# Kernel tuning notes

Measured on AMD Instinct MI355X. Metric: run time of the kernel, lower is better.

## Reference

```python
import jax, jax.numpy as jnp
import numpy as np

B = 8192
INPUT_DIM = 1024
PATH_DIM = 256
HIDDEN_DIM = 1024
OUTPUT_DIM = 1024
STEPS = 50


def setup_inputs() -> dict:
    key = jax.random.key(0)
    ks = jax.random.split(key, 12)
    s = lambda fan_in: 1.0 / np.sqrt(fan_in)
    x0 = jax.random.normal(ks[0], (B, INPUT_DIM), dtype=jnp.float32)
    W_pe = jax.random.uniform(ks[1], (INPUT_DIM, PATH_DIM), jnp.float32, -s(INPUT_DIM), s(INPUT_DIM))
    b_pe = jax.random.uniform(ks[2], (PATH_DIM,), jnp.float32, -s(INPUT_DIM), s(INPUT_DIM))
    W_hi = jax.random.uniform(ks[3], (INPUT_DIM, HIDDEN_DIM), jnp.float32, -s(INPUT_DIM), s(INPUT_DIM))
    b_hi = jax.random.uniform(ks[4], (HIDDEN_DIM,), jnp.float32, -s(INPUT_DIM), s(INPUT_DIM))
    f_in = HIDDEN_DIM + PATH_DIM
    W1 = jax.random.uniform(ks[5], (f_in, HIDDEN_DIM), jnp.float32, -s(f_in), s(f_in))
    b1 = jax.random.uniform(ks[6], (HIDDEN_DIM,), jnp.float32, -s(f_in), s(f_in))
    W2 = jax.random.uniform(ks[7], (HIDDEN_DIM, HIDDEN_DIM), jnp.float32, -s(HIDDEN_DIM), s(HIDDEN_DIM))
    b2 = jax.random.uniform(ks[8], (HIDDEN_DIM,), jnp.float32, -s(HIDDEN_DIM), s(HIDDEN_DIM))
    W_ro = jax.random.uniform(ks[9], (HIDDEN_DIM, OUTPUT_DIM), jnp.float32, -s(HIDDEN_DIM), s(HIDDEN_DIM))
    b_ro = jax.random.uniform(ks[10], (OUTPUT_DIM,), jnp.float32, -s(HIDDEN_DIM), s(HIDDEN_DIM))
    return {"x0": x0, "W_pe": W_pe, "b_pe": b_pe, "W_hi": W_hi, "b_hi": b_hi,
            "W1": W1, "b1": b1, "W2": W2, "b2": b2, "W_ro": W_ro, "b_ro": b_ro}


def reference(x0, W_pe, b_pe, W_hi, b_hi, W1, b1, W2, b2, W_ro, b_ro):
    dt = 1.0 / float(STEPS)
    g = x0 @ W_pe + b_pe          # [B, path_dim]
    z0 = x0 @ W_hi + b_hi          # [B, hidden_dim]
    ts = dt * jnp.arange(1, STEPS + 1, dtype=jnp.float32)  # t after each step

    def step(z, t):
        u_t = t * g                                  # [B, path_dim]
        inp = jnp.concatenate([z, u_t], axis=-1)     # [B, hidden+path]
        dz = jnp.tanh(inp @ W1 + b1) @ W2 + b2       # [B, hidden_dim]
        return z + dt * dz, None

    z, _ = jax.lax.scan(step, z0, ts)
    return z @ W_ro + b_ro
```

## Files before the change

### kernel.cpp

```cpp
#include <hip/hip_runtime.h>
#include <hip/hip_bf16.h>

typedef __hip_bfloat16 bf16;
typedef __bf16 bf16x8 __attribute__((ext_vector_type(8)));
typedef float f32x4 __attribute__((ext_vector_type(4)));

#define ROWS   32
#define HID    1024
#define PATH   256
#define NSTEP  50
#define P      1032
#define SMEM_BYTES (2 * ROWS * P * 2)

__device__ __forceinline__ f32x4 mfma16(bf16x8 a, bf16x8 b, f32x4 c) {
    return __builtin_amdgcn_mfma_f32_16x16x32_bf16(a, b, c, 0, 0, 0);
}

__device__ __forceinline__ float tanh_fast(float x) {
    float e = __expf(2.0f * x);
    return 1.0f - 2.0f / (e + 1.0f);
}

__device__ __forceinline__ bf16x8 ldcvt8(const float* __restrict__ p) {
    f32x4 lo = *(const f32x4*)p;
    f32x4 hi = *(const f32x4*)(p + 4);
    bf16x8 r;
    #pragma unroll
    for (int j = 0; j < 4; j++) { r[j] = (__bf16)lo[j]; r[4 + j] = (__bf16)hi[j]; }
    return r;
}

__global__ void pack_frag(const float* __restrict__ src, bf16* __restrict__ dst, int N) {
    int kb = blockIdx.x, nb = blockIdx.y, l = threadIdx.x;
    int lm = l & 15, lq = l >> 4;
    bf16x8 v;
    #pragma unroll
    for (int j = 0; j < 8; j++)
        v[j] = __float2bfloat16(src[(size_t)(kb * 32 + lq * 8 + j) * N + nb * 16 + lm]);
    *(bf16x8*)(dst + ((size_t)(kb * gridDim.y + nb) * 64 + l) * 8) = v;
}

template<int KB>
__device__ __forceinline__ void gemm4r(const bf16* __restrict__ lds,
                                       const bf16* __restrict__ Wp,
                                       int wave, int lane, int rot, f32x4 (&acc)[2][4]) {
    const int lm = lane & 15, lq = lane >> 4;
    #pragma unroll 2
    for (int kb = 0; kb < KB; kb++) {
        int kbr = kb + rot; if (kbr >= KB) kbr -= KB;
        const bf16* wp = Wp + (((size_t)kbr * 64 + wave * 4) * 64 + lane) * 8;
        bf16x8 w[4];
        #pragma unroll
        for (int nt = 0; nt < 4; nt++) w[nt] = *(const bf16x8*)(wp + nt * 512);
        bf16x8 a0 = *(const bf16x8*)(lds + lm * P + kbr * 32 + lq * 8);
        bf16x8 a1 = *(const bf16x8*)(lds + (16 + lm) * P + kbr * 32 + lq * 8);
        #pragma unroll
        for (int nt = 0; nt < 4; nt++) {
            acc[0][nt] = mfma16(a0, w[nt], acc[0][nt]);
            acc[1][nt] = mfma16(a1, w[nt], acc[1][nt]);
        }
    }
}

__global__ __launch_bounds__(1024) void cde_main(
    const float* __restrict__ x0,  const float* __restrict__ b_pe, const float* __restrict__ b_hi,
    const float* __restrict__ b1v, const float* __restrict__ b2v,  const float* __restrict__ b_ro,
    const bf16* __restrict__ WpeP, const bf16* __restrict__ WhiP,
    const bf16* __restrict__ W1zP, const bf16* __restrict__ W1uP,
    const bf16* __restrict__ W2P,  const bf16* __restrict__ WroP,
    float* __restrict__ out)
{
    extern __shared__ bf16 smem[];
    bf16* inp = smem;
    bf16* th  = smem + ROWS * P;

    const int tid  = threadIdx.x;
    const int wave = tid >> 6;
    const int lane = tid & 63;
    const int lm   = lane & 15;
    const int lq   = lane >> 4;
    const int rot  = (blockIdx.x >> 3) & 31;
    const long row0 = (long)blockIdx.x * ROWS;

    f32x4 z[2][4];
    f32x4 g[2];
    f32x4 c_u[2][4];

    #pragma unroll
    for (int nt = 0; nt < 4; nt++) {
        float b = b_hi[wave * 64 + nt * 16 + lm];
        #pragma unroll
        for (int r = 0; r < 4; r++) { z[0][nt][r] = b; z[1][nt][r] = b; }
    }
    {
        float b = b_pe[wave * 16 + lm];
        #pragma unroll
        for (int r = 0; r < 4; r++) { g[0][r] = b; g[1][r] = b; }
    }
    for (int kb = 0; kb < HID / 32; kb++) {
        int kbr = kb + rot; if (kbr >= 32) kbr -= 32;
        bf16x8 a0 = ldcvt8(x0 + (row0 +      lm) * HID + kbr * 32 + lq * 8);
        bf16x8 a1 = ldcvt8(x0 + (row0 + 16 + lm) * HID + kbr * 32 + lq * 8);
        const bf16* wp = WhiP + (((size_t)kbr * 64 + wave * 4) * 64 + lane) * 8;
        #pragma unroll
        for (int nt = 0; nt < 4; nt++) {
            bf16x8 bb = *(const bf16x8*)(wp + nt * 512);
            z[0][nt] = mfma16(a0, bb, z[0][nt]);
            z[1][nt] = mfma16(a1, bb, z[1][nt]);
        }
        bf16x8 pb = *(const bf16x8*)(WpeP + (((size_t)kbr * 16 + wave) * 64 + lane) * 8);
        g[0] = mfma16(a0, pb, g[0]);
        g[1] = mfma16(a1, pb, g[1]);
    }

    #pragma unroll
    for (int mt = 0; mt < 2; mt++)
        #pragma unroll
        for (int r = 0; r < 4; r++)
            inp[(mt * 16 + lq * 4 + r) * P + wave * 16 + lm] = __float2bfloat16(g[mt][r]);
    __syncthreads();
    #pragma unroll
    for (int mt = 0; mt < 2; mt++)
        #pragma unroll
        for (int nt = 0; nt < 4; nt++)
            #pragma unroll
            for (int r = 0; r < 4; r++) c_u[mt][nt][r] = 0.0f;
    for (int kb = 0; kb < PATH / 32; kb++) {
        const bf16* wp = W1uP + (((size_t)kb * 64 + wave * 4) * 64 + lane) * 8;
        bf16x8 a0 = *(const bf16x8*)(inp + lm * P + kb * 32 + lq * 8);
        bf16x8 a1 = *(const bf16x8*)(inp + (16 + lm) * P + kb * 32 + lq * 8);
        #pragma unroll
        for (int nt = 0; nt < 4; nt++) {
            bf16x8 bb = *(const bf16x8*)(wp + nt * 512);
            c_u[0][nt] = mfma16(a0, bb, c_u[0][nt]);
            c_u[1][nt] = mfma16(a1, bb, c_u[1][nt]);
        }
    }
    __syncthreads();

    float b1r[4], b2r[4];
    #pragma unroll
    for (int nt = 0; nt < 4; nt++) {
        b1r[nt] = b1v[wave * 64 + nt * 16 + lm];
        b2r[nt] = b2v[wave * 64 + nt * 16 + lm];
    }

    const float DT = 1.0f / (float)NSTEP;

    for (int s = 0; s < NSTEP; s++) {
        float t = DT * (float)(s + 1);

        #pragma unroll
        for (int mt = 0; mt < 2; mt++)
            #pragma unroll
            for (int nt = 0; nt < 4; nt++)
                #pragma unroll
                for (int r = 0; r < 4; r++)
                    inp[(mt * 16 + lq * 4 + r) * P + wave * 64 + nt * 16 + lm] =
                        __float2bfloat16(z[mt][nt][r]);
        __syncthreads();

        {
            f32x4 acc[2][4];
            #pragma unroll
            for (int mt = 0; mt < 2; mt++)
                #pragma unroll
                for (int nt = 0; nt < 4; nt++)
                    #pragma unroll
                    for (int r = 0; r < 4; r++)
                        acc[mt][nt][r] = fmaf(t, c_u[mt][nt][r], b1r[nt]);
            gemm4r<HID / 32>(inp, W1zP, wave, lane, rot, acc);
            #pragma unroll
            for (int mt = 0; mt < 2; mt++)
                #pragma unroll
                for (int nt = 0; nt < 4; nt++)
                    #pragma unroll
                    for (int r = 0; r < 4; r++)
                        th[(mt * 16 + lq * 4 + r) * P + wave * 64 + nt * 16 + lm] =
                            __float2bfloat16(tanh_fast(acc[mt][nt][r]));
        }
        __syncthreads();

        {
            f32x4 acc[2][4];
            #pragma unroll
            for (int nt = 0; nt < 4; nt++)
                #pragma unroll
                for (int r = 0; r < 4; r++) { acc[0][nt][r] = b2r[nt]; acc[1][nt][r] = b2r[nt]; }
            gemm4r<HID / 32>(th, W2P, wave, lane, rot, acc);
            #pragma unroll
            for (int mt = 0; mt < 2; mt++)
                #pragma unroll
                for (int nt = 0; nt < 4; nt++)
                    #pragma unroll
                    for (int r = 0; r < 4; r++)
                        z[mt][nt][r] += DT * acc[mt][nt][r];
        }
    }

    #pragma unroll
    for (int mt = 0; mt < 2; mt++)
        #pragma unroll
        for (int nt = 0; nt < 4; nt++)
            #pragma unroll
            for (int r = 0; r < 4; r++)
                inp[(mt * 16 + lq * 4 + r) * P + wave * 64 + nt * 16 + lm] =
                    __float2bfloat16(z[mt][nt][r]);
    __syncthreads();
    {
        f32x4 acc[2][4];
        #pragma unroll
        for (int nt = 0; nt < 4; nt++) {
            float b = b_ro[wave * 64 + nt * 16 + lm];
            #pragma unroll
            for (int r = 0; r < 4; r++) { acc[0][nt][r] = b; acc[1][nt][r] = b; }
        }
        gemm4r<HID / 32>(inp, WroP, wave, lane, rot, acc);
        #pragma unroll
        for (int mt = 0; mt < 2; mt++)
            #pragma unroll
            for (int nt = 0; nt < 4; nt++)
                #pragma unroll
                for (int r = 0; r < 4; r++)
                    out[(row0 + mt * 16 + lq * 4 + r) * HID + wave * 64 + nt * 16 + lm] =
                        acc[mt][nt][r];
    }
}

extern "C" void kernel_launch(void* const* d_in, const int* in_sizes, int n_in,
                              void* d_out, int out_size, void* d_ws, size_t ws_size,
                              hipStream_t stream) {
    (void)in_sizes; (void)n_in; (void)out_size; (void)ws_size;
    const float* x0  = (const float*)d_in[0];
    const float* Wpe = (const float*)d_in[1];
    const float* bpe = (const float*)d_in[2];
    const float* Whi = (const float*)d_in[3];
    const float* bhi = (const float*)d_in[4];
    const float* W1  = (const float*)d_in[5];
    const float* b1  = (const float*)d_in[6];
    const float* W2  = (const float*)d_in[7];
    const float* b2  = (const float*)d_in[8];
    const float* Wro = (const float*)d_in[9];
    const float* bro = (const float*)d_in[10];

    bf16* ws   = (bf16*)d_ws;
    bf16* WpeP = ws;
    bf16* WhiP = WpeP + 256 * 1024;
    bf16* W1zP = WhiP + 1024 * 1024;
    bf16* W1uP = W1zP + 1024 * 1024;
    bf16* W2P  = W1uP + 256 * 1024;
    bf16* WroP = W2P  + 1024 * 1024;

    hipLaunchKernelGGL(pack_frag, dim3(1024 / 32, 256 / 16), dim3(64), 0, stream, Wpe, WpeP, 256);
    hipLaunchKernelGGL(pack_frag, dim3(1024 / 32, 1024 / 16), dim3(64), 0, stream, Whi, WhiP, 1024);
    hipLaunchKernelGGL(pack_frag, dim3(1024 / 32, 1024 / 16), dim3(64), 0, stream, W1, W1zP, 1024);
    hipLaunchKernelGGL(pack_frag, dim3(256 / 32, 1024 / 16), dim3(64), 0, stream,
                       W1 + (size_t)1024 * 1024, W1uP, 1024);
    hipLaunchKernelGGL(pack_frag, dim3(1024 / 32, 1024 / 16), dim3(64), 0, stream, W2, W2P, 1024);
    hipLaunchKernelGGL(pack_frag, dim3(1024 / 32, 1024 / 16), dim3(64), 0, stream, Wro, WroP, 1024);

    hipFuncSetAttribute((const void*)cde_main,
                        hipFuncAttributeMaxDynamicSharedMemorySize, SMEM_BYTES);
    hipLaunchKernelGGL(cde_main, dim3(8192 / ROWS), dim3(1024), SMEM_BYTES, stream,
                       x0, bpe, bhi, b1, b2, bro, WpeP, WhiP, W1zP, W1uP, W2P, WroP,
                       (float*)d_out);
}
```

Measured before the change: 3.057 ms.

## Software-pipeline GEMM loads, pack constants to bf16, fold DT into tanh to cut registers

```diff
diff --git a/kernel.cpp b/kernel.cpp
--- a/kernel.cpp
+++ b/kernel.cpp
@@ -30,6 +30,17 @@
     return r;
 }
 
+__device__ __forceinline__ unsigned bfbits(float f) {
+    __hip_bfloat16 h = __float2bfloat16(f);
+    unsigned short u; __builtin_memcpy(&u, &h, 2);
+    return (unsigned)u;
+}
+__device__ __forceinline__ unsigned bfpack2(float lo, float hi) {
+    return bfbits(lo) | (bfbits(hi) << 16);
+}
+__device__ __forceinline__ float bflo(unsigned u) { return __uint_as_float(u << 16); }
+__device__ __forceinline__ float bfhi(unsigned u) { return __uint_as_float(u & 0xffff0000u); }
+
 __global__ void pack_frag(const float* __restrict__ src, bf16* __restrict__ dst, int N) {
     int kb = blockIdx.x, nb = blockIdx.y, l = threadIdx.x;
     int lm = l & 15, lq = l >> 4;
@@ -41,28 +52,67 @@
 }
 
 template<int KB>
-__device__ __forceinline__ void gemm4r(const bf16* __restrict__ lds,
+__device__ __forceinline__ void gemm4p(const bf16* __restrict__ lds,
                                        const bf16* __restrict__ Wp,
                                        int wave, int lane, int rot, f32x4 (&acc)[2][4]) {
+    static_assert((KB & (KB - 1)) == 0, "KB must be a power of two");
     const int lm = lane & 15, lq = lane >> 4;
+    const bf16* a0b = lds + lm * P + lq * 8;
+    const bf16* a1b = a0b + 16 * P;
+    const int woff = wave * 2048 + lane * 8;
+
+    bf16x8 w[4], a0A, a1A, a0B, a1B;
+    {
+        const int k0 = rot & (KB - 1);
+        const int k1 = (rot + 1) & (KB - 1);
+        const bf16* wp = Wp + (size_t)k0 * 32768 + woff;
+        #pragma unroll
+        for (int nt = 0; nt < 4; nt++) w[nt] = *(const bf16x8*)(wp + nt * 512);
+        a0A = *(const bf16x8*)(a0b + k0 * 32);
+        a1A = *(const bf16x8*)(a1b + k0 * 32);
+        a0B = *(const bf16x8*)(a0b + k1 * 32);
+        a1B = *(const bf16x8*)(a1b + k1 * 32);
+    }
     #pragma unroll 2
-    for (int kb = 0; kb < KB; kb++) {
-        int kbr = kb + rot; if (kbr >= KB) kbr -= KB;
-        const bf16* wp = Wp + (((size_t)kbr * 64 + wave * 4) * 64 + lane) * 8;
-        bf16x8 w[4];
-        #pragma unroll
-        for (int nt = 0; nt < 4; nt++) w[nt] = *(const bf16x8*)(wp + nt * 512);
-        bf16x8 a0 = *(const bf16x8*)(lds + lm * P + kbr * 32 + lq * 8);
-        bf16x8 a1 = *(const bf16x8*)(lds + (16 + lm) * P + kbr * 32 + lq * 8);
-        #pragma unroll
-        for (int nt = 0; nt < 4; nt++) {
-            acc[0][nt] = mfma16(a0, w[nt], acc[0][nt]);
-            acc[1][nt] = mfma16(a1, w[nt], acc[1][nt]);
-        }
-    }
-}
-
-__global__ __launch_bounds__(1024) void cde_main(
+    for (int kb = 0; kb < KB; kb += 2) {
+        const int kw1 = (kb + 1 + rot) & (KB - 1);
+        const int ka1 = (kb + 2 + rot) & (KB - 1);
+        const bf16* wp1 = Wp + (size_t)kw1 * 32768 + woff;
+        acc[0][0] = mfma16(a0A, w[0], acc[0][0]);
+        acc[1][0] = mfma16(a1A, w[0], acc[1][0]);
+        w[0] = *(const bf16x8*)(wp1);
+        acc[0][1] = mfma16(a0A, w[1], acc[0][1]);
+        acc[1][1] = mfma16(a1A, w[1], acc[1][1]);
+        w[1] = *(const bf16x8*)(wp1 + 512);
+        acc[0][2] = mfma16(a0A, w[2], acc[0][2]);
+        acc[1][2] = mfma16(a1A, w[2], acc[1][2]);
+        w[2] = *(const bf16x8*)(wp1 + 1024);
+        acc[0][3] = mfma16(a0A, w[3], acc[0][3]);
+        acc[1][3] = mfma16(a1A, w[3], acc[1][3]);
+        w[3] = *(const bf16x8*)(wp1 + 1536);
+        a0A = *(const bf16x8*)(a0b + ka1 * 32);
+        a1A = *(const bf16x8*)(a1b + ka1 * 32);
+        const int kw2 = ka1;
+        const int ka2 = (kb + 3 + rot) & (KB - 1);
+        const bf16* wp2 = Wp + (size_t)kw2 * 32768 + woff;
+        acc[0][0] = mfma16(a0B, w[0], acc[0][0]);
+        acc[1][0] = mfma16(a1B, w[0], acc[1][0]);
+        w[0] = *(const bf16x8*)(wp2);
+        acc[0][1] = mfma16(a0B, w[1], acc[0][1]);
+        acc[1][1] = mfma16(a1B, w[1], acc[1][1]);
+        w[1] = *(const bf16x8*)(wp2 + 512);
+        acc[0][2] = mfma16(a0B, w[2], acc[0][2]);
+        acc[1][2] = mfma16(a1B, w[2], acc[1][2]);
+        w[2] = *(const bf16x8*)(wp2 + 1024);
+        acc[0][3] = mfma16(a0B, w[3], acc[0][3]);
+        acc[1][3] = mfma16(a1B, w[3], acc[1][3]);
+        w[3] = *(const bf16x8*)(wp2 + 1536);
+        a0B = *(const bf16x8*)(a0b + ka2 * 32);
+        a1B = *(const bf16x8*)(a1b + ka2 * 32);
+    }
+}
+
+__global__ __launch_bounds__(1024, 4) void cde_main(
     const float* __restrict__ x0,  const float* __restrict__ b_pe, const float* __restrict__ b_hi,
     const float* __restrict__ b1v, const float* __restrict__ b2v,  const float* __restrict__ b_ro,
     const bf16* __restrict__ WpeP, const bf16* __restrict__ WhiP,
@@ -84,7 +134,7 @@
 
     f32x4 z[2][4];
     f32x4 g[2];
-    f32x4 c_u[2][4];
+    uint2 cu_pk[2][4];
 
     #pragma unroll
     for (int nt = 0; nt < 4; nt++) {
@@ -119,33 +169,41 @@
         for (int r = 0; r < 4; r++)
             inp[(mt * 16 + lq * 4 + r) * P + wave * 16 + lm] = __float2bfloat16(g[mt][r]);
     __syncthreads();
-    #pragma unroll
-    for (int mt = 0; mt < 2; mt++)
-        #pragma unroll
-        for (int nt = 0; nt < 4; nt++)
-            #pragma unroll
-            for (int r = 0; r < 4; r++) c_u[mt][nt][r] = 0.0f;
-    for (int kb = 0; kb < PATH / 32; kb++) {
-        const bf16* wp = W1uP + (((size_t)kb * 64 + wave * 4) * 64 + lane) * 8;
-        bf16x8 a0 = *(const bf16x8*)(inp + lm * P + kb * 32 + lq * 8);
-        bf16x8 a1 = *(const bf16x8*)(inp + (16 + lm) * P + kb * 32 + lq * 8);
-        #pragma unroll
-        for (int nt = 0; nt < 4; nt++) {
-            bf16x8 bb = *(const bf16x8*)(wp + nt * 512);
-            c_u[0][nt] = mfma16(a0, bb, c_u[0][nt]);
-            c_u[1][nt] = mfma16(a1, bb, c_u[1][nt]);
-        }
+    {
+        f32x4 cu[2][4];
+        #pragma unroll
+        for (int mt = 0; mt < 2; mt++)
+            #pragma unroll
+            for (int nt = 0; nt < 4; nt++)
+                #pragma unroll
+                for (int r = 0; r < 4; r++) cu[mt][nt][r] = 0.0f;
+        for (int kb = 0; kb < PATH / 32; kb++) {
+            const bf16* wp = W1uP + (((size_t)kb * 64 + wave * 4) * 64 + lane) * 8;
+            bf16x8 a0 = *(const bf16x8*)(inp + lm * P + kb * 32 + lq * 8);
+            bf16x8 a1 = *(const bf16x8*)(inp + (16 + lm) * P + kb * 32 + lq * 8);
+            #pragma unroll
+            for (int nt = 0; nt < 4; nt++) {
+                bf16x8 bb = *(const bf16x8*)(wp + nt * 512);
+                cu[0][nt] = mfma16(a0, bb, cu[0][nt]);
+                cu[1][nt] = mfma16(a1, bb, cu[1][nt]);
+            }
+        }
+        #pragma unroll
+        for (int mt = 0; mt < 2; mt++)
+            #pragma unroll
+            for (int nt = 0; nt < 4; nt++)
+                cu_pk[mt][nt] = make_uint2(bfpack2(cu[mt][nt][0], cu[mt][nt][1]),
+                                           bfpack2(cu[mt][nt][2], cu[mt][nt][3]));
     }
     __syncthreads();
 
-    float b1r[4], b2r[4];
-    #pragma unroll
-    for (int nt = 0; nt < 4; nt++) {
-        b1r[nt] = b1v[wave * 64 + nt * 16 + lm];
-        b2r[nt] = b2v[wave * 64 + nt * 16 + lm];
-    }
-
     const float DT = 1.0f / (float)NSTEP;
+
+    unsigned b12[4];
+    #pragma unroll
+    for (int nt = 0; nt < 4; nt++)
+        b12[nt] = bfpack2(b1v[wave * 64 + nt * 16 + lm],
+                          DT * b2v[wave * 64 + nt * 16 + lm]);
 
     for (int s = 0; s < NSTEP; s++) {
         float t = DT * (float)(s + 1);
@@ -165,11 +223,15 @@
             #pragma unroll
             for (int mt = 0; mt < 2; mt++)
                 #pragma unroll
-                for (int nt = 0; nt < 4; nt++)
-                    #pragma unroll
-                    for (int r = 0; r < 4; r++)
-                        acc[mt][nt][r] = fmaf(t, c_u[mt][nt][r], b1r[nt]);
-            gemm4r<HID / 32>(inp, W1zP, wave, lane, rot, acc);
+                for (int nt = 0; nt < 4; nt++) {
+                    float b1 = bflo(b12[nt]);
+                    unsigned px = cu_pk[mt][nt].x, py = cu_pk[mt][nt].y;
+                    acc[mt][nt][0] = fmaf(t, bflo(px), b1);
+                    acc[mt][nt][1] = fmaf(t, bfhi(px), b1);
+                    acc[mt][nt][2] = fmaf(t, bflo(py), b1);
+                    acc[mt][nt][3] = fmaf(t, bfhi(py), b1);
+                }
+            gemm4p<HID / 32>(inp, W1zP, wave, lane, rot, acc);
             #pragma unroll
             for (int mt = 0; mt < 2; mt++)
                 #pragma unroll
@@ -177,24 +239,20 @@
                     #pragma unroll
                     for (int r = 0; r < 4; r++)
                         th[(mt * 16 + lq * 4 + r) * P + wave * 64 + nt * 16 + lm] =
-                            __float2bfloat16(tanh_fast(acc[mt][nt][r]));
+                            __float2bfloat16(DT * tanh_fast(acc[mt][nt][r]));
         }
         __syncthreads();
 
         {
-            f32x4 acc[2][4];
-            #pragma unroll
-            for (int nt = 0; nt < 4; nt++)
-                #pragma unroll
-                for (int r = 0; r < 4; r++) { acc[0][nt][r] = b2r[nt]; acc[1][nt][r] = b2r[nt]; }
-            gemm4r<HID / 32>(th, W2P, wave, lane, rot, acc);
             #pragma unroll
             for (int mt = 0; mt < 2; mt++)
                 #pragma unroll
-                for (int nt = 0; nt < 4; nt++)
+                for (int nt = 0; nt < 4; nt++) {
+                    float db = bfhi(b12[nt]);
                     #pragma unroll
-                    for (int r = 0; r < 4; r++)
-                        z[mt][nt][r] += DT * acc[mt][nt][r];
+                    for (int r = 0; r < 4; r++) z[mt][nt][r] += db;
+                }
+            gemm4p<HID / 32>(th, W2P, wave, lane, rot, z);
         }
     }
 
@@ -215,7 +273,7 @@
             #pragma unroll
             for (int r = 0; r < 4; r++) { acc[0][nt][r] = b; acc[1][nt][r] = b; }
         }
-        gemm4r<HID / 32>(inp, WroP, wave, lane, rot, acc);
+        gemm4p<HID / 32>(inp, WroP, wave, lane, rot, acc);
         #pragma unroll
         for (int mt = 0; mt < 2; mt++)
             #pragma unroll
```

Result: faster. 2.631 ms (-13.9%).
